# Optimization experiments

Hardware: AMD Instinct MI355X
Metric: run time of the kernel (lower is better)

Reference implementation:

```python
import jax, jax.numpy as jnp
import numpy as np

NUM_HEADS = 16
EPS = 1e-6  # LinearAttention.epsilon

def setup_inputs() -> dict:
    key = jax.random.key(0)
    ks = jax.random.split(key, 10)
    B, L, D = 4, 4096, 2048
    s = 1.0 / np.sqrt(D)
    x = jax.random.normal(ks[0], (B, L, D), dtype=jnp.float32)
    attention_mask = jnp.ones((B, L), dtype=jnp.float32)
    Wq = jax.random.normal(ks[1], (D, D), dtype=jnp.float32) * s
    bq = jnp.zeros((D,), dtype=jnp.float32)
    Wk = jax.random.normal(ks[2], (D, D), dtype=jnp.float32) * s
    bk = jnp.zeros((D,), dtype=jnp.float32)
    Wv = jax.random.normal(ks[3], (D, D), dtype=jnp.float32) * s
    bv = jnp.zeros((D,), dtype=jnp.float32)
    Wo = jax.random.normal(ks[4], (D, D), dtype=jnp.float32) * s
    bo = jnp.zeros((D,), dtype=jnp.float32)
    return {"x": x, "attention_mask": attention_mask, "Wq": Wq, "bq": bq,
            "Wk": Wk, "bk": bk, "Wv": Wv, "bv": bv, "Wo": Wo, "bo": bo}

def reference(x, attention_mask, Wq, bq, Wk, bk, Wv, bv, Wo, bo):
    B, L, Dm = x.shape
    H = NUM_HEADS
    Dh = Dm // H
    # q/k/v projections -> [B, H, L, Dh]
    def proj(W, b):
        return (x @ W + b).reshape(B, L, H, Dh).transpose(0, 2, 1, 3)
    q = proj(Wq, bq)
    k = proj(Wk, bk)
    v = proj(Wv, bv)
    # feature map: elu(x) + 1
    q = jax.nn.elu(q) + 1.0
    k = jax.nn.elu(k) + 1.0
    # mask keys/values: mask [B, 1, L, 1]
    m = attention_mask[:, None, :, None]
    k = k * m
    v = v * m
    # causal linear attention via cumulative sums over sequence dim
    k_cum = jnp.cumsum(k, axis=2)          # [B,H,L,Dh]
    kv_cum = jnp.cumsum(k * v, axis=2)     # [B,H,L,Dh] (diagonal kv state, as in source)
    z = jnp.sum(q * k_cum, axis=-1) + EPS  # [B,H,L]
    z = z * attention_mask[:, None, :]
    out = (q * kv_cum) / z[..., None]      # [B,H,L,Dh]
    out = out.transpose(0, 2, 1, 3).reshape(B, L, Dm)
    return out @ Wo + bo
```

## Files before the change

kernel.cpp:

```cpp
#include <hip/hip_runtime.h>
#include <cstdint>
#include <cstddef>

#define EPS_F 1e-6f

__device__ inline unsigned short f2bf(float f) {
    union { float f; unsigned u; } v; v.f = f;
    unsigned r = v.u + 0x7fffu + ((v.u >> 16) & 1u);
    return (unsigned short)(r >> 16);
}
__device__ inline float bf2f(unsigned u16) {
    union { unsigned u; float f; } v; v.u = u16 << 16; return v.f;
}

typedef __attribute__((ext_vector_type(8))) __bf16 bf16x8;
typedef __attribute__((ext_vector_type(8))) short short8;
typedef __attribute__((ext_vector_type(8))) unsigned short ushort8;
typedef __attribute__((ext_vector_type(4))) float floatx4;
typedef __attribute__((ext_vector_type(4))) unsigned uintx4;

__device__ inline void async_load16(const void* g, void* l) {
    __builtin_amdgcn_global_load_lds((const __attribute__((address_space(1))) void*)g,
                                     (__attribute__((address_space(3))) void*)l,
                                     16, 0, 0);
}

#define LDS_OFF(p) ((unsigned)(unsigned long long)(const __attribute__((address_space(3))) void*)(p))

__global__ void cast_x_kernel(const float* __restrict__ in, unsigned short* __restrict__ out, int n8) {
    int i = blockIdx.x * blockDim.x + threadIdx.x;
    if (i < n8) {
        float4 a = ((const float4*)in)[2 * i];
        float4 b = ((const float4*)in)[2 * i + 1];
        short8 o;
        o[0] = (short)f2bf(a.x); o[1] = (short)f2bf(a.y);
        o[2] = (short)f2bf(a.z); o[3] = (short)f2bf(a.w);
        o[4] = (short)f2bf(b.x); o[5] = (short)f2bf(b.y);
        o[6] = (short)f2bf(b.z); o[7] = (short)f2bf(b.w);
        ((short8*)out)[i] = o;
    }
}

__global__ void transpose_cast_kernel(const float* __restrict__ W0, const float* __restrict__ W1,
                                      const float* __restrict__ W2, const float* __restrict__ W3,
                                      unsigned short* __restrict__ WtBase, int n) {
    const float* W = (blockIdx.z == 0) ? W0 : (blockIdx.z == 1) ? W1 : (blockIdx.z == 2) ? W2 : W3;
    unsigned short* Wt = WtBase + (size_t)blockIdx.z * n * n;
    __shared__ float tile[32][33];
    int bx = blockIdx.x * 32;
    int by = blockIdx.y * 32;
    int tx = threadIdx.x;
    int ty = threadIdx.y;
    #pragma unroll
    for (int i = 0; i < 32; i += 8)
        tile[ty + i][tx] = W[(size_t)(by + ty + i) * n + bx + tx];
    __syncthreads();
    #pragma unroll
    for (int i = 0; i < 32; i += 8)
        Wt[(size_t)(bx + ty + i) * n + by + tx] = f2bf(tile[tx][ty + i]);
}

#define BMT 128
#define BNT 128
#define BKT 64
#define DMODEL 2048

__global__ __launch_bounds__(256, 2)
void gemm_qkv(const unsigned short* __restrict__ A,
              const unsigned short* __restrict__ Bt,
              const float* __restrict__ b0, const float* __restrict__ b1,
              const float* __restrict__ b2,
              const float* __restrict__ mask,
              unsigned short* __restrict__ qo, unsigned short* __restrict__ ko,
              unsigned short* __restrict__ vo,
              int M, int K) {
    __shared__ __align__(16) unsigned short As[BMT * BKT];
    __shared__ __align__(16) unsigned short Bs[BNT * BKT];

    const int tid  = threadIdx.x;
    const int wave = tid >> 6;
    const int lane = tid & 63;
    const int m0    = blockIdx.x * BMT;
    const int nglob = blockIdx.y * BNT;
    const int mat  = nglob >> 11;
    const int n0   = nglob & (DMODEL - 1);
    const float* bias = (mat == 0) ? b0 : (mat == 1) ? b1 : b2;
    unsigned short* Cb = (mat == 0) ? qo : (mat == 1) ? ko : vo;

    const int wm = (wave >> 1) * 64;
    const int wn = (wave & 1) * 64;
    const int quad  = lane >> 4;
    const int row16 = lane & 15;

    floatx4 acc[4][4] = {};

    const int srow_lo = lane >> 3;
    const int schunk  = lane & 7;

    for (int k0 = 0; k0 < K; k0 += BKT) {
        #pragma unroll
        for (int i = 0; i < 4; i++) {
            int slot_base = wave * 256 + i * 64;
            int r  = wave * 32 + i * 8 + srow_lo;
            int cg = schunk ^ (r & 7);
            const unsigned short* ga = A  + (size_t)(m0 + r) * K + k0 + cg * 8;
            const unsigned short* gb = Bt + (size_t)(nglob + r) * K + k0 + cg * 8;
            async_load16(ga, As + (size_t)slot_base * 8);
            async_load16(gb, Bs + (size_t)slot_base * 8);
        }
        __syncthreads();

        #pragma unroll
        for (int kk = 0; kk < 2; kk++) {
            bf16x8 af[4], bfr[4];
            #pragma unroll
            for (int t = 0; t < 4; t++) {
                int ra = wm + t * 16 + row16;
                int ca = (kk * 4 + quad) ^ (ra & 7);
                af[t]  = __builtin_bit_cast(bf16x8, *(const short8*)(As + (size_t)ra * 64 + ca * 8));
                int rb = wn + t * 16 + row16;
                int cb = (kk * 4 + quad) ^ (rb & 7);
                bfr[t] = __builtin_bit_cast(bf16x8, *(const short8*)(Bs + (size_t)rb * 64 + cb * 8));
            }
            #pragma unroll
            for (int i = 0; i < 4; i++)
                #pragma unroll
                for (int j = 0; j < 4; j++)
                    acc[i][j] = __builtin_amdgcn_mfma_f32_16x16x32_bf16(af[i], bfr[j], acc[i][j], 0, 0, 0);
        }
        __syncthreads();
    }

    float bcache[4];
    #pragma unroll
    for (int j = 0; j < 4; j++) bcache[j] = bias[n0 + wn + j * 16 + row16];
    #pragma unroll
    for (int i = 0; i < 4; i++) {
        #pragma unroll
        for (int r = 0; r < 4; r++) {
            int row = m0 + wm + i * 16 + quad * 4 + r;
            float mr = (mat >= 1) ? mask[row] : 1.0f;
            #pragma unroll
            for (int j = 0; j < 4; j++) {
                int col = n0 + wn + j * 16 + row16;
                float v = acc[i][j][r] + bcache[j];
                if (mat <= 1) v = (v > 0.f) ? (v + 1.f) : __expf(v);
                v *= mr;
                Cb[(size_t)row * DMODEL + col] = f2bf(v);
            }
        }
    }
}

#define FBK 32
#define FSLOT_ELEMS (256 * FBK)
#define FSLOT_BYTES 16384

#define DSR(dst, base, OFF) \
    asm volatile("ds_read_b128 %0, %1 offset:" OFF : "=v"(dst) : "v"(base) : "memory")
#define READ_A0(f, base) { DSR(f[0], base, "0");    DSR(f[1], base, "1024"); \
                           DSR(f[2], base, "2048"); DSR(f[3], base, "3072"); }
#define READ_A1(f, base) { DSR(f[0], base, "4096"); DSR(f[1], base, "5120"); \
                           DSR(f[2], base, "6144"); DSR(f[3], base, "7168"); }
#define READ_B(f, base)  { DSR(f[0], base, "0");    DSR(f[1], base, "1024"); \
                           DSR(f[2], base, "2048"); DSR(f[3], base, "3072"); }

#define MFMA_HALF(i0, af, bf)                                                   \
    _Pragma("unroll")                                                           \
    for (int i_ = 0; i_ < 4; i_++) {                                            \
        bf16x8 a_ = __builtin_bit_cast(bf16x8, af[i_]);                         \
        _Pragma("unroll")                                                       \
        for (int j_ = 0; j_ < 4; j_++)                                          \
            acc[i0 + i_][j_] = __builtin_amdgcn_mfma_f32_16x16x32_bf16(         \
                a_, __builtin_bit_cast(bf16x8, bf[j_]), acc[i0 + i_][j_], 0, 0, 0); \
    }

#define GEMM_ITER(T, BCUR, BNXT)                                                \
  {                                                                             \
    const int T_ = (T);                                                         \
    if (T_ <= NT - 3)      asm volatile("s_waitcnt vmcnt(4)" ::: "memory");     \
    else if (T_ == NT - 2) asm volatile("s_waitcnt vmcnt(0)" ::: "memory");     \
    __builtin_amdgcn_s_barrier();                                               \
    __builtin_amdgcn_sched_barrier(0);                                          \
    if (T_ + 3 < NT) stage(T_ + 3, (T_ + 3) & 3);                               \
    asm volatile("s_waitcnt lgkmcnt(4)" ::: "memory");                          \
    __builtin_amdgcn_sched_barrier(0);                                          \
    __builtin_amdgcn_s_setprio(1);                                              \
    MFMA_HALF(0, af0, BCUR);                                                    \
    __builtin_amdgcn_s_setprio(0);                                              \
    const int tn_ = T_ + 1;                                                     \
    const unsigned aN_ = aLane + (unsigned)((tn_ & 3) * FSLOT_BYTES);           \
    const unsigned bN_ = bLane + (unsigned)((tn_ & 3) * FSLOT_BYTES);           \
    if (tn_ < NT) {                                                             \
      READ_A0(af0, aN_);                                                        \
      READ_B(BNXT, bN_);                                                        \
      asm volatile("s_waitcnt lgkmcnt(8)" ::: "memory");                        \
    } else {                                                                    \
      asm volatile("s_waitcnt lgkmcnt(0)" ::: "memory");                        \
    }                                                                           \
    __builtin_amdgcn_sched_barrier(0);                                          \
    __builtin_amdgcn_s_setprio(1);                                              \
    MFMA_HALF(4, af1, BCUR);                                                    \
    __builtin_amdgcn_s_setprio(0);                                              \
    if (tn_ < NT) { READ_A1(af1, aN_); }                                        \
  }

__global__ __launch_bounds__(512, 2)
void gemm_final(const unsigned short* __restrict__ A,
                const unsigned short* __restrict__ Bt,
                const float* __restrict__ bias,
                float* __restrict__ Cf,
                int M, int K) {
    __shared__ __align__(16) unsigned short As[4 * FSLOT_ELEMS];
    __shared__ __align__(16) unsigned short Bs[4 * FSLOT_ELEMS];

    const int tid  = threadIdx.x;
    const int lane = tid & 63;
    const int wave = tid >> 6;
    const int wr   = wave >> 2;
    const int wc   = wave & 3;
    const int quad  = lane >> 4;
    const int row16 = lane & 15;

    const int nwg = (int)(gridDim.x * gridDim.y);
    const int bid = (int)(blockIdx.y * gridDim.x + blockIdx.x);
    const int cpx = nwg >> 3;
    const int swz = (bid & 7) * cpx + (bid >> 3);
    const int bm  = swz % (int)gridDim.x;
    const int bn  = swz / (int)gridDim.x;

    const int m0 = bm * 256;
    const int n0 = bn * 256;

    floatx4 acc[8][4] = {};

    const unsigned short* gA[2];
    const unsigned short* gB[2];
    #pragma unroll
    for (int b = 0; b < 2; b++) {
        int s = b * 512 + tid;
        int r = s >> 2, c = s & 3;
        int cg = c ^ ((r >> 1) & 3);
        gA[b] = A  + (size_t)(m0 + r) * K + cg * 8;
        gB[b] = Bt + (size_t)(n0 + r) * K + cg * 8;
    }

    const unsigned asB = LDS_OFF(As);
    const unsigned bsB = LDS_OFF(Bs);
    const unsigned cP    = (unsigned)(quad ^ ((row16 >> 1) & 3));
    const unsigned aLane = asB + (unsigned)(wr * 8192 + row16 * 64) + cP * 16u;
    const unsigned bLane = bsB + (unsigned)(wc * 4096 + row16 * 64) + cP * 16u;

    auto stage = [&](int tt, int sl) {
        const int koff = tt * FBK;
        #pragma unroll
        for (int b = 0; b < 2; b++) {
            int s = b * 512 + tid;
            async_load16(gA[b] + koff, As + sl * FSLOT_ELEMS + s * 8);
            async_load16(gB[b] + koff, Bs + sl * FSLOT_ELEMS + s * 8);
        }
    };

    const int NT = K / FBK;
    stage(0, 0); stage(1, 1); stage(2, 2);
    asm volatile("s_waitcnt vmcnt(8)" ::: "memory");
    __builtin_amdgcn_s_barrier();
    __builtin_amdgcn_sched_barrier(0);

    uintx4 af0[4], af1[4], bfE[4], bfO[4];
    READ_A0(af0, aLane);
    READ_B(bfE, bLane);
    READ_A1(af1, aLane);

    for (int t = 0; t < NT; t += 2) {
        GEMM_ITER(t,     bfE, bfO);
        GEMM_ITER(t + 1, bfO, bfE);
    }

    float bcache[4];
    #pragma unroll
    for (int j = 0; j < 4; j++) bcache[j] = bias[n0 + wc * 64 + j * 16 + row16];
    #pragma unroll
    for (int i = 0; i < 8; i++) {
        #pragma unroll
        for (int r = 0; r < 4; r++) {
            int row = m0 + wr * 128 + i * 16 + quad * 4 + r;
            #pragma unroll
            for (int j = 0; j < 4; j++) {
                int col = n0 + wc * 64 + j * 16 + row16;
                Cf[(size_t)row * DMODEL + col] = acc[i][j][r] + bcache[j];
            }
        }
    }
}

#define SL    4096
#define SD    2048
#define SH    16
#define CHUNK 64
#define NCH   64

__global__ void scan_partial_kernel(const unsigned short* __restrict__ k,
                                    const unsigned short* __restrict__ v,
                                    float* __restrict__ sumK, float* __restrict__ sumKV) {
    int blk = blockIdx.x;
    int c = blk & (NCH - 1), bh = blk >> 6;
    int b = bh >> 4, h = bh & (SH - 1);
    int lane = threadIdx.x;
    int tg = lane >> 4, dg = lane & 15;
    size_t base = ((size_t)(b * SL + c * CHUNK + tg)) * SD + h * 128 + dg * 8;
    float sk[8] = {0.f, 0.f, 0.f, 0.f, 0.f, 0.f, 0.f, 0.f};
    float skv[8] = {0.f, 0.f, 0.f, 0.f, 0.f, 0.f, 0.f, 0.f};
    for (int it = 0; it < CHUNK / 4; it++) {
        ushort8 kw = *(const ushort8*)(k + base);
        ushort8 vw = *(const ushort8*)(v + base);
        #pragma unroll
        for (int j = 0; j < 8; j++) {
            float kf = bf2f(kw[j]);
            float vf = bf2f(vw[j]);
            sk[j] += kf; skv[j] += kf * vf;
        }
        base += (size_t)4 * SD;
    }
    #pragma unroll
    for (int j = 0; j < 8; j++) {
        sk[j]  += __shfl_xor(sk[j], 16);  sk[j]  += __shfl_xor(sk[j], 32);
        skv[j] += __shfl_xor(skv[j], 16); skv[j] += __shfl_xor(skv[j], 32);
    }
    if (tg == 0) {
        size_t o = ((size_t)bh * NCH + c) * 128 + dg * 8;
        *(float4*)(sumK  + o)     = make_float4(sk[0], sk[1], sk[2], sk[3]);
        *(float4*)(sumK  + o + 4) = make_float4(sk[4], sk[5], sk[6], sk[7]);
        *(float4*)(sumKV + o)     = make_float4(skv[0], skv[1], skv[2], skv[3]);
        *(float4*)(sumKV + o + 4) = make_float4(skv[4], skv[5], skv[6], skv[7]);
    }
}

__global__ __launch_bounds__(64)
void scan_offsets_kernel(const float* __restrict__ sumK, const float* __restrict__ sumKV,
                         float* __restrict__ offK, float* __restrict__ offKV) {
    int blk = blockIdx.x;
    int bh  = blk >> 1;
    int d   = (blk & 1) * 64 + threadIdx.x;
    float aK = 0.f, aKV = 0.f;
    #pragma unroll 1
    for (int h = 0; h < 2; h++) {
        float vK[32], vKV[32];
        #pragma unroll
        for (int c2 = 0; c2 < 32; c2++) {
            size_t o = ((size_t)bh * NCH + h * 32 + c2) * 128 + d;
            vK[c2] = sumK[o]; vKV[c2] = sumKV[o];
        }
        #pragma unroll
        for (int c2 = 0; c2 < 32; c2++) {
            size_t o = ((size_t)bh * NCH + h * 32 + c2) * 128 + d;
            offK[o]  = aK;  aK  += vK[c2];
            offKV[o] = aKV; aKV += vKV[c2];
        }
    }
}

__global__ void scan_final_kernel(const unsigned short* __restrict__ q,
                                  const unsigned short* __restrict__ k,
                                  const unsigned short* __restrict__ v,
                                  const float* __restrict__ offK, const float* __restrict__ offKV,
                                  const float* __restrict__ mask,
                                  unsigned short* __restrict__ out) {
    int blk = blockIdx.x;
    int c   = blk & (NCH - 1);
    int bhp = blk >> 6;
    int b = bhp >> 3, hp = bhp & 7;
    int lane = threadIdx.x;
    int half = lane >> 5, dq = lane & 31;
    int h  = hp * 2 + half;
    int bh = b * SH + h;

    size_t ob = ((size_t)bh * NCH + c) * 128 + dq * 4;
    float4 kc4 = *(const float4*)(offK  + ob);
    float4 kv4 = *(const float4*)(offKV + ob);
    float kc[4] = {kc4.x, kc4.y, kc4.z, kc4.w};
    float kv[4] = {kv4.x, kv4.y, kv4.z, kv4.w};

    size_t base = ((size_t)(b * SL + c * CHUNK)) * SD + h * 128 + dq * 4;
    const float* mrow = mask + (size_t)b * SL + c * CHUNK;

    for (int s = 0; s < CHUNK / 4; s++) {
        uint2 kw[4], vw[4], qw[4];
        #pragma unroll
        for (int u = 0; u < 4; u++) {
            size_t a = base + (size_t)u * SD;
            kw[u] = *(const uint2*)(k + a);
            vw[u] = *(const uint2*)(v + a);
            qw[u] = *(const uint2*)(q + a);
        }
        float p[4], nn[4][4];
        #pragma unroll
        for (int u = 0; u < 4; u++) {
            float kf[4], vf[4], qf[4];
            kf[0] = bf2f(kw[u].x & 0xffff); kf[1] = bf2f(kw[u].x >> 16);
            kf[2] = bf2f(kw[u].y & 0xffff); kf[3] = bf2f(kw[u].y >> 16);
            vf[0] = bf2f(vw[u].x & 0xffff); vf[1] = bf2f(vw[u].x >> 16);
            vf[2] = bf2f(vw[u].y & 0xffff); vf[3] = bf2f(vw[u].y >> 16);
            qf[0] = bf2f(qw[u].x & 0xffff); qf[1] = bf2f(qw[u].x >> 16);
            qf[2] = bf2f(qw[u].y & 0xffff); qf[3] = bf2f(qw[u].y >> 16);
            float pu = 0.f;
            #pragma unroll
            for (int j = 0; j < 4; j++) {
                kc[j] += kf[j];
                kv[j] += kf[j] * vf[j];
                pu += qf[j] * kc[j];
                nn[u][j] = qf[j] * kv[j];
            }
            p[u] = pu;
        }
        #pragma unroll
        for (int off = 16; off > 0; off >>= 1) {
            #pragma unroll
            for (int u = 0; u < 4; u++) p[u] += __shfl_xor(p[u], off);
        }
        #pragma unroll
        for (int u = 0; u < 4; u++) {
            float z = (p[u] + EPS_F) * mrow[s * 4 + u];
            float inv = 1.0f / z;
            uint2 o2;
            unsigned lo0 = f2bf(nn[u][0] * inv), hi0 = f2bf(nn[u][1] * inv);
            unsigned lo1 = f2bf(nn[u][2] * inv), hi1 = f2bf(nn[u][3] * inv);
            o2.x = lo0 | (hi0 << 16);
            o2.y = lo1 | (hi1 << 16);
            *(uint2*)(out + base + (size_t)u * SD) = o2;
        }
        base += (size_t)4 * SD;
    }
}

extern "C" void kernel_launch(void* const* d_in, const int* in_sizes, int n_in,
                              void* d_out, int out_size, void* d_ws, size_t ws_size,
                              hipStream_t stream) {
    const float* x  = (const float*)d_in[0];
    const float* am = (const float*)d_in[1];
    const float* Wq = (const float*)d_in[2];
    const float* bq = (const float*)d_in[3];
    const float* Wk = (const float*)d_in[4];
    const float* bk = (const float*)d_in[5];
    const float* Wv = (const float*)d_in[6];
    const float* bv = (const float*)d_in[7];
    const float* Wo = (const float*)d_in[8];
    const float* bo = (const float*)d_in[9];
    float* out = (float*)d_out;

    const int Bb = 4, L = 4096, D = 2048;
    const int M = Bb * L;
    const size_t MD = (size_t)M * D;

    char* w = (char*)d_ws;
    unsigned short* xb    = (unsigned short*)w; w += MD * 2;
    unsigned short* qb    = (unsigned short*)w; w += MD * 2;
    unsigned short* kb    = (unsigned short*)w; w += MD * 2;
    unsigned short* vb    = (unsigned short*)w; w += MD * 2;
    unsigned short* WT    = (unsigned short*)w; w += (size_t)4 * D * D * 2;
    float* sumK  = (float*)w; w += (size_t)64 * NCH * 128 * 4;
    float* sumKV = (float*)w; w += (size_t)64 * NCH * 128 * 4;
    float* offK  = (float*)w; w += (size_t)64 * NCH * 128 * 4;
    float* offKV = (float*)w; w += (size_t)64 * NCH * 128 * 4;
    unsigned short* attnb = xb;

    int n8 = (int)(MD / 8);
    cast_x_kernel<<<(n8 + 255) / 256, 256, 0, stream>>>(x, xb, n8);
    dim3 tb(32, 8);
    dim3 tg(D / 32, D / 32, 4);
    transpose_cast_kernel<<<tg, tb, 0, stream>>>(Wq, Wk, Wv, Wo, WT, D);

    dim3 gq(M / BMT, 3 * D / BNT);
    gemm_qkv<<<gq, 256, 0, stream>>>(xb, WT, bq, bk, bv, am, qb, kb, vb, M, D);

    scan_partial_kernel<<<64 * NCH, 64, 0, stream>>>(kb, vb, sumK, sumKV);
    scan_offsets_kernel<<<128, 64, 0, stream>>>(sumK, sumKV, offK, offKV);
    scan_final_kernel<<<2048, 64, 0, stream>>>(qb, kb, vb, offK, offKV, am, attnb);

    dim3 go(M / 256, D / 256);
    gemm_final<<<go, 512, 0, stream>>>(attnb, WT + (size_t)3 * D * D, bo, out, M, D);
}
```

Baseline: 896.2 us.

## Rewrite QKV projection GEMM with 256x256 tiles and multi-stage pipelined LDS loads

Replaces the simple single-buffered 128x128 QKV GEMM with the same 4-slot, 256x256-tile, 512-thread software-pipelined design already used by the output GEMM. Global-to-LDS async loads for later k-tiles are issued ahead while MFMAs run on the current tile, and LDS fragment reads are interleaved with compute. The aim is to hide memory latency and raise data reuse in the largest GEMM. It uses more LDS and registers per block, which may reduce occupancy, and the larger tiles give fewer blocks.

Measured after the change: 878.6 us. About the same (-2.0%).

```diff
diff --git a/kernel.cpp b/kernel.cpp
--- a/kernel.cpp
+++ b/kernel.cpp
@@ -60,98 +60,7 @@
         Wt[(size_t)(bx + ty + i) * n + by + tx] = f2bf(tile[tx][ty + i]);
 }
 
-#define BMT 128
-#define BNT 128
-#define BKT 64
 #define DMODEL 2048
-
-__global__ __launch_bounds__(256, 2)
-void gemm_qkv(const unsigned short* __restrict__ A,
-              const unsigned short* __restrict__ Bt,
-              const float* __restrict__ b0, const float* __restrict__ b1,
-              const float* __restrict__ b2,
-              const float* __restrict__ mask,
-              unsigned short* __restrict__ qo, unsigned short* __restrict__ ko,
-              unsigned short* __restrict__ vo,
-              int M, int K) {
-    __shared__ __align__(16) unsigned short As[BMT * BKT];
-    __shared__ __align__(16) unsigned short Bs[BNT * BKT];
-
-    const int tid  = threadIdx.x;
-    const int wave = tid >> 6;
-    const int lane = tid & 63;
-    const int m0    = blockIdx.x * BMT;
-    const int nglob = blockIdx.y * BNT;
-    const int mat  = nglob >> 11;
-    const int n0   = nglob & (DMODEL - 1);
-    const float* bias = (mat == 0) ? b0 : (mat == 1) ? b1 : b2;
-    unsigned short* Cb = (mat == 0) ? qo : (mat == 1) ? ko : vo;
-
-    const int wm = (wave >> 1) * 64;
-    const int wn = (wave & 1) * 64;
-    const int quad  = lane >> 4;
-    const int row16 = lane & 15;
-
-    floatx4 acc[4][4] = {};
-
-    const int srow_lo = lane >> 3;
-    const int schunk  = lane & 7;
-
-    for (int k0 = 0; k0 < K; k0 += BKT) {
-        #pragma unroll
-        for (int i = 0; i < 4; i++) {
-            int slot_base = wave * 256 + i * 64;
-            int r  = wave * 32 + i * 8 + srow_lo;
-            int cg = schunk ^ (r & 7);
-            const unsigned short* ga = A  + (size_t)(m0 + r) * K + k0 + cg * 8;
-            const unsigned short* gb = Bt + (size_t)(nglob + r) * K + k0 + cg * 8;
-            async_load16(ga, As + (size_t)slot_base * 8);
-            async_load16(gb, Bs + (size_t)slot_base * 8);
-        }
-        __syncthreads();
-
-        #pragma unroll
-        for (int kk = 0; kk < 2; kk++) {
-            bf16x8 af[4], bfr[4];
-            #pragma unroll
-            for (int t = 0; t < 4; t++) {
-                int ra = wm + t * 16 + row16;
-                int ca = (kk * 4 + quad) ^ (ra & 7);
-                af[t]  = __builtin_bit_cast(bf16x8, *(const short8*)(As + (size_t)ra * 64 + ca * 8));
-                int rb = wn + t * 16 + row16;
-                int cb = (kk * 4 + quad) ^ (rb & 7);
-                bfr[t] = __builtin_bit_cast(bf16x8, *(const short8*)(Bs + (size_t)rb * 64 + cb * 8));
-            }
-            #pragma unroll
-            for (int i = 0; i < 4; i++)
-                #pragma unroll
-                for (int j = 0; j < 4; j++)
-                    acc[i][j] = __builtin_amdgcn_mfma_f32_16x16x32_bf16(af[i], bfr[j], acc[i][j], 0, 0, 0);
-        }
-        __syncthreads();
-    }
-
-    float bcache[4];
-    #pragma unroll
-    for (int j = 0; j < 4; j++) bcache[j] = bias[n0 + wn + j * 16 + row16];
-    #pragma unroll
-    for (int i = 0; i < 4; i++) {
-        #pragma unroll
-        for (int r = 0; r < 4; r++) {
-            int row = m0 + wm + i * 16 + quad * 4 + r;
-            float mr = (mat >= 1) ? mask[row] : 1.0f;
-            #pragma unroll
-            for (int j = 0; j < 4; j++) {
-                int col = n0 + wn + j * 16 + row16;
-                float v = acc[i][j][r] + bcache[j];
-                if (mat <= 1) v = (v > 0.f) ? (v + 1.f) : __expf(v);
-                v *= mr;
-                Cb[(size_t)row * DMODEL + col] = f2bf(v);
-            }
-        }
-    }
-}
-
 #define FBK 32
 #define FSLOT_ELEMS (256 * FBK)
 #define FSLOT_BYTES 16384
@@ -206,6 +115,99 @@
   }
 
 __global__ __launch_bounds__(512, 2)
+void gemm_qkv(const unsigned short* __restrict__ A,
+              const unsigned short* __restrict__ Bt,
+              const float* __restrict__ b0, const float* __restrict__ b1,
+              const float* __restrict__ b2,
+              const float* __restrict__ mask,
+              unsigned short* __restrict__ qo, unsigned short* __restrict__ ko,
+              unsigned short* __restrict__ vo,
+              int M, int K) {
+    __shared__ __align__(16) unsigned short As[4 * FSLOT_ELEMS];
+    __shared__ __align__(16) unsigned short Bs[4 * FSLOT_ELEMS];
+
+    const int tid  = threadIdx.x;
+    const int lane = tid & 63;
+    const int wave = tid >> 6;
+    const int wr   = wave >> 2;
+    const int wc   = wave & 3;
+    const int quad  = lane >> 4;
+    const int row16 = lane & 15;
+
+    const int m0    = blockIdx.x * 256;
+    const int nglob = blockIdx.y * 256;
+    const int mat = nglob >> 11;
+    const int n0  = nglob & (DMODEL - 1);
+    const float* bias = (mat == 0) ? b0 : (mat == 1) ? b1 : b2;
+    unsigned short* Cb = (mat == 0) ? qo : (mat == 1) ? ko : vo;
+
+    floatx4 acc[8][4] = {};
+
+    const unsigned short* gA[2];
+    const unsigned short* gB[2];
+    #pragma unroll
+    for (int b = 0; b < 2; b++) {
+        int s = b * 512 + tid;
+        int r = s >> 2, c = s & 3;
+        int cg = c ^ ((r >> 1) & 3);
+        gA[b] = A  + (size_t)(m0 + r) * K + cg * 8;
+        gB[b] = Bt + (size_t)(nglob + r) * K + cg * 8;
+    }
+
+    const unsigned asB = LDS_OFF(As);
+    const unsigned bsB = LDS_OFF(Bs);
+    const unsigned cP    = (unsigned)(quad ^ ((row16 >> 1) & 3));
+    const unsigned aLane = asB + (unsigned)(wr * 8192 + row16 * 64) + cP * 16u;
+    const unsigned bLane = bsB + (unsigned)(wc * 4096 + row16 * 64) + cP * 16u;
+
+    auto stage = [&](int tt, int sl) {
+        const int koff = tt * FBK;
+        #pragma unroll
+        for (int b = 0; b < 2; b++) {
+            int s = b * 512 + tid;
+            async_load16(gA[b] + koff, As + sl * FSLOT_ELEMS + s * 8);
+            async_load16(gB[b] + koff, Bs + sl * FSLOT_ELEMS + s * 8);
+        }
+    };
+
+    const int NT = K / FBK;
+    stage(0, 0); stage(1, 1); stage(2, 2);
+    asm volatile("s_waitcnt vmcnt(8)" ::: "memory");
+    __builtin_amdgcn_s_barrier();
+    __builtin_amdgcn_sched_barrier(0);
+
+    uintx4 af0[4], af1[4], bfE[4], bfO[4];
+    READ_A0(af0, aLane);
+    READ_B(bfE, bLane);
+    READ_A1(af1, aLane);
+
+    for (int t = 0; t < NT; t += 2) {
+        GEMM_ITER(t,     bfE, bfO);
+        GEMM_ITER(t + 1, bfO, bfE);
+    }
+
+    float bcache[4];
+    #pragma unroll
+    for (int j = 0; j < 4; j++) bcache[j] = bias[n0 + wc * 64 + j * 16 + row16];
+    #pragma unroll
+    for (int i = 0; i < 8; i++) {
+        #pragma unroll
+        for (int r = 0; r < 4; r++) {
+            int row = m0 + wr * 128 + i * 16 + quad * 4 + r;
+            float mr = (mat >= 1) ? mask[row] : 1.0f;
+            #pragma unroll
+            for (int j = 0; j < 4; j++) {
+                int col = n0 + wc * 64 + j * 16 + row16;
+                float v = acc[i][j][r] + bcache[j];
+                if (mat <= 1) v = (v > 0.f) ? (v + 1.f) : __expf(v);
+                v *= mr;
+                Cb[(size_t)row * DMODEL + col] = f2bf(v);
+            }
+        }
+    }
+}
+
+__global__ __launch_bounds__(512, 2)
 void gemm_final(const unsigned short* __restrict__ A,
                 const unsigned short* __restrict__ Bt,
                 const float* __restrict__ bias,
@@ -470,8 +472,8 @@
     dim3 tg(D / 32, D / 32, 4);
     transpose_cast_kernel<<<tg, tb, 0, stream>>>(Wq, Wk, Wv, Wo, WT, D);
 
-    dim3 gq(M / BMT, 3 * D / BNT);
-    gemm_qkv<<<gq, 256, 0, stream>>>(xb, WT, bq, bk, bv, am, qb, kb, vb, M, D);
+    dim3 gq(M / 256, 3 * D / 256);
+    gemm_qkv<<<gq, 512, 0, stream>>>(xb, WT, bq, bk, bv, am, qb, kb, vb, M, D);
 
     scan_partial_kernel<<<64 * NCH, 64, 0, stream>>>(kb, vb, sumK, sumKV);
     scan_offsets_kernel<<<128, 64, 0, stream>>>(sumK, sumKV, offK, offKV);
```
